# Optimization experiments

Hardware: AMD Instinct MI355X
Metric: run time of the kernel (lower is better)

Reference implementation:

```python
import jax, jax.numpy as jnp
import numpy as np

FEATURE_DIM = 512
Z_DIM = 256
Q_DIM = 128
NUM_Z_CODES = 4096
NUM_Q_CODES = 2048
HIDDEN_DIM = 128 * 4  # 512
BOTTLENECK = 64
BATCH = 32768


def setup_inputs() -> dict:
    key = jax.random.key(0)
    ks = jax.random.split(key, 16)
    d = {}
    d['x'] = jax.random.normal(ks[0], (BATCH, FEATURE_DIM), dtype=jnp.float32)
    # encoder: Linear(feature_dim,64) -> GELU -> Linear(64,hidden) -> GELU
    d['eW1'] = jax.random.normal(ks[1], (BOTTLENECK, FEATURE_DIM), dtype=jnp.float32) * (1.0 / np.sqrt(FEATURE_DIM))
    d['eb1'] = jnp.zeros((BOTTLENECK,), jnp.float32)
    d['eW2'] = jax.random.normal(ks[2], (HIDDEN_DIM, BOTTLENECK), dtype=jnp.float32) * (1.0 / np.sqrt(BOTTLENECK))
    d['eb2'] = jnp.zeros((HIDDEN_DIM,), jnp.float32)
    # to_z_latent LipschitzMLP(hidden, z_dim)
    d['zW'] = jax.random.normal(ks[3], (Z_DIM, HIDDEN_DIM), dtype=jnp.float32) * (1.0 / np.sqrt(HIDDEN_DIM))
    d['zb'] = jnp.zeros((Z_DIM,), jnp.float32)
    d['zci'] = jnp.ones((Z_DIM,), jnp.float32)
    # z codebook
    d['z_codebook'] = jax.random.normal(ks[4], (NUM_Z_CODES, Z_DIM), dtype=jnp.float32)
    # q_encoder LipschitzMLP(z_dim, q_dim)
    d['qW'] = jax.random.normal(ks[5], (Q_DIM, Z_DIM), dtype=jnp.float32) * (1.0 / np.sqrt(Z_DIM))
    d['qb'] = jnp.zeros((Q_DIM,), jnp.float32)
    d['qci'] = jnp.ones((Q_DIM,), jnp.float32)
    # q codebook
    d['q_codebook'] = jax.random.normal(ks[6], (NUM_Q_CODES, Q_DIM), dtype=jnp.float32)
    # decoder: Linear(q_dim,64) -> GELU -> Linear(64,hidden) -> GELU
    d['dW1'] = jax.random.normal(ks[7], (BOTTLENECK, Q_DIM), dtype=jnp.float32) * (1.0 / np.sqrt(Q_DIM))
    d['db1'] = jnp.zeros((BOTTLENECK,), jnp.float32)
    d['dW2'] = jax.random.normal(ks[8], (HIDDEN_DIM, BOTTLENECK), dtype=jnp.float32) * (1.0 / np.sqrt(BOTTLENECK))
    d['db2'] = jnp.zeros((HIDDEN_DIM,), jnp.float32)
    # to_output Linear(hidden, feature_dim)
    d['oW'] = jax.random.normal(ks[9], (FEATURE_DIM, HIDDEN_DIM), dtype=jnp.float32) * (1.0 / np.sqrt(HIDDEN_DIM))
    d['ob'] = jnp.zeros((FEATURE_DIM,), jnp.float32)
    return d


def _gelu(x):
    return jax.nn.gelu(x, approximate=False)  # torch nn.GELU default (erf)


def _lipschitz_mlp(x, W, b, ci):
    # normalization: scale each row of W so its L1 norm <= softplus(ci)
    absrowsum = jnp.sum(jnp.abs(W), axis=1, keepdims=True)          # [out,1]
    scale = jnp.minimum(1.0, jax.nn.softplus(ci)[:, None] / absrowsum)
    W_norm = W * scale
    return jax.nn.sigmoid(x @ W_norm.T + b)


def _quantize(z_e, codebook):
    # ||a-b||^2 = ||a||^2 + ||b||^2 - 2 a.b ; single big GEMM
    z_norm = jnp.sum(z_e * z_e, axis=1, keepdims=True)              # [B,1]
    cb_norm = jnp.sum(codebook * codebook, axis=1)[None, :]         # [1,K]
    dists = z_norm + cb_norm - 2.0 * (z_e @ codebook.T)             # [B,K]
    idx = jnp.argmin(dists, axis=1)
    z_q = codebook[idx]
    return z_q, idx


def _mse(a, b):
    return jnp.mean((a - b) ** 2)


def reference(x, eW1, eb1, eW2, eb2, zW, zb, zci, z_codebook,
              qW, qb, qci, q_codebook, dW1, db1, dW2, db2, oW, ob):
    sg = jax.lax.stop_gradient
    # encoder
    h = _gelu(_gelu(x @ eW1.T + eb1) @ eW2.T + eb2)                 # [B,hidden]
    z_e = _lipschitz_mlp(h, zW, zb, zci)                            # [B,z_dim]
    z_q, z_idx = _quantize(z_e, z_codebook)
    commit_z = _mse(z_e, sg(z_q))
    codebook_z = _mse(z_q, sg(z_e))
    # q level
    q_e = _lipschitz_mlp(sg(z_q), qW, qb, qci)                      # [B,q_dim]
    q_q, q_idx = _quantize(q_e, q_codebook)
    commit_q = _mse(q_e, sg(q_q))
    codebook_q = _mse(q_q, sg(q_e))
    # decoder
    dec_h = _gelu(_gelu(q_q @ dW1.T + db1) @ dW2.T + db2)           # [B,hidden]
    x_recon = dec_h @ oW.T + ob                                     # [B,feature]
    recon_loss = _mse(x_recon, x)
    loss = recon_loss + 0.25 * (commit_z + codebook_z) + 0.25 * (commit_q + codebook_q)
    return (loss, recon_loss, commit_z, codebook_z, commit_q, codebook_q,
            x_recon, z_q, q_q, z_idx, q_idx)
```

## Files before the change

### kernel.cpp

```cpp
#include <hip/hip_runtime.h>

typedef unsigned long long u64;
typedef unsigned short u16;
typedef unsigned int u32;


namespace {

constexpr int kBatch = 32768;

__device__ __forceinline__ float gelu_f(float x) {
  return 0.5f * x * (1.0f + erff(x * 0.70710678118654752440f));
}
__device__ __forceinline__ float sigmoid_f(float x) {
  return 1.0f / (1.0f + expf(-x));
}
__device__ __forceinline__ u64 pack_key(float d, unsigned j) {
  unsigned u = __float_as_uint(d);
  u = (u & 0x80000000u) ? ~u : (u | 0x80000000u);
  return ((u64)u << 32) | j;
}
__device__ __forceinline__ u16 bf16_rne(float x) {
  unsigned u = __float_as_uint(x);
  unsigned r = (u + 0x7FFFu + ((u >> 16) & 1u)) >> 16;
  return (u16)r;
}
__device__ __forceinline__ float bf16_to_f(u16 h) {
  return __uint_as_float((unsigned)h << 16);
}
__device__ __forceinline__ u64 min64(u64 a, u64 b) { return a < b ? a : b; }

__device__ __forceinline__ void load_lds16(const void* g, void* l) {
  __builtin_amdgcn_global_load_lds(
      (const __attribute__((address_space(1))) void*)g,
      (__attribute__((address_space(3))) void*)l, 16, 0, 0);
}

typedef short bf16x8 __attribute__((ext_vector_type(8)));
typedef float f32x4 __attribute__((ext_vector_type(4)));

__global__ void prep_cb_kernel(const float* __restrict__ zcb,
                               u16* __restrict__ zcbh, float* __restrict__ zcbn,
                               const float* __restrict__ qcb,
                               u16* __restrict__ qcbh, float* __restrict__ qcbn) {
  int b = blockIdx.x;
  const float* cb;
  u16* cbh;
  float* cbn;
  int K;
  if (b < 1024) { cb = zcb; cbh = zcbh; cbn = zcbn; K = 256; }
  else { b -= 1024; cb = qcb; cbh = qcbh; cbn = qcbn; K = 128; }
  const int row = b * 4 + (threadIdx.x >> 6);
  const int lane = threadIdx.x & 63;
  double s = 0.0;
  for (int k = lane; k < K; k += 64) {
    const float v = cb[(size_t)row * K + k];
    cbh[(size_t)row * K + k] = bf16_rne(v);
    s += (double)v * (double)v;
  }
#pragma unroll
  for (int o = 32; o > 0; o >>= 1) s += __shfl_down(s, o);
  if (lane == 0) cbn[row] = (float)s;
}

__global__ void prep_w_kernel(
    const float* __restrict__ zW, const float* __restrict__ zci,
    const float* __restrict__ qW, const float* __restrict__ qci,
    const float* __restrict__ eW1, const float* __restrict__ eW2,
    u16* __restrict__ zWns, u16* __restrict__ qWns, u16* __restrict__ eW1s,
    u16* __restrict__ eW2s, const float* __restrict__ dW1,
    const float* __restrict__ dW2, const float* __restrict__ oW,
    u16* __restrict__ dW1b, u16* __restrict__ dW2b, u16* __restrict__ oWb) {
  const int b = blockIdx.x;
  const int tid = threadIdx.x;
  if (b < 384) {
    const float* W;
    const float* ci;
    u16* D;
    int K, row;
    if (b < 256) { W = zW; ci = zci; D = zWns; K = 512; row = b; }
    else { W = qW; ci = qci; D = qWns; K = 256; row = b - 256; }
    float s = 0.f;
    for (int k = tid; k < K; k += 256) s += fabsf(W[(size_t)row * K + k]);
#pragma unroll
    for (int o = 32; o > 0; o >>= 1) s += __shfl_down(s, o);
    __shared__ float p[4];
    if ((tid & 63) == 0) p[tid >> 6] = s;
    __syncthreads();
    const float tot = p[0] + p[1] + p[2] + p[3];
    const float c = ci[row];
    const float sp = (c > 20.f) ? c : log1pf(expf(c));
    const float scale = fminf(1.f, sp / tot);
    for (int k = tid; k < K; k += 256) {
      const float v = W[(size_t)row * K + k] * scale;
      const u16 h = bf16_rne(v);
      const u16 l = bf16_rne(v - bf16_to_f(h));
      D[(size_t)row * 3 * K + k] = h;
      D[(size_t)row * 3 * K + K + k] = h;
      D[(size_t)row * 3 * K + 2 * K + k] = l;
    }
  } else if (b < 512) {
    const int i = (b - 384) * 256 + tid;
    const int r = i >> 9, k = i & 511;
    const float v = eW1[i];
    const u16 h = bf16_rne(v);
    const u16 l = bf16_rne(v - bf16_to_f(h));
    eW1s[(size_t)r * 1536 + k] = h;
    eW1s[(size_t)r * 1536 + 512 + k] = h;
    eW1s[(size_t)r * 1536 + 1024 + k] = l;
  } else if (b < 640) {
    const int i = (b - 512) * 256 + tid;
    const int r = i >> 6, k = i & 63;
    const float v = eW2[i];
    const u16 h = bf16_rne(v);
    const u16 l = bf16_rne(v - bf16_to_f(h));
    eW2s[(size_t)r * 192 + k] = h;
    eW2s[(size_t)r * 192 + 64 + k] = h;
    eW2s[(size_t)r * 192 + 128 + k] = l;
  } else if (b < 672) {
    const int i = (b - 640) * 256 + tid;
    dW1b[i] = bf16_rne(dW1[i]);
  } else if (b < 800) {
    const int i = (b - 672) * 256 + tid;
    dW2b[i] = bf16_rne(dW2[i]);
  } else {
    const int i = (b - 800) * 256 + tid;
    oWb[i] = bf16_rne(oW[i]);
  }
}

__global__ void cast_split_x_kernel(const float* __restrict__ x,
                                    u16* __restrict__ xs) {
  const int i = blockIdx.x * 256 + threadIdx.x;
  const int row = i >> 7, c4 = i & 127;
  const float4 v = *(const float4*)(x + (size_t)row * 512 + c4 * 4);
  const float vv[4] = {v.x, v.y, v.z, v.w};
  u16 hv[4], lv[4];
#pragma unroll
  for (int j = 0; j < 4; ++j) {
    hv[j] = bf16_rne(vv[j]);
    lv[j] = bf16_rne(vv[j] - bf16_to_f(hv[j]));
  }
  *(ushort4*)(xs + (size_t)row * 1024 + c4 * 4) =
      make_ushort4(hv[0], hv[1], hv[2], hv[3]);
  *(ushort4*)(xs + (size_t)row * 1024 + 512 + c4 * 4) =
      make_ushort4(lv[0], lv[1], lv[2], lv[3]);
}

enum { U_GELU_SPLIT = 0, U_SIG_SPLIT = 1, U_GELU_B16 = 2, U_RECON = 3 };

template <int TM, int TN, int NW, int MODE>
__global__ __launch_bounds__(NW * 64) void gemm_uni(
    const u16* __restrict__ A, const u16* __restrict__ B,
    const float* __restrict__ bias, void* __restrict__ Cv,
    const float* __restrict__ X, float* __restrict__ sumptr, int Ktot,
    int wrapA, int strideA, int N) {
  __shared__ __align__(16) u16 As[TM * 64];
  __shared__ __align__(16) u16 Bs[TN * 64];
  constexpr int NT = NW * 64;
  constexpr int AIT = (TM * 8) / NT;
  constexpr int BIT = (TN * 8) / NT;
  const int tid = threadIdx.x;
  const int lane = tid & 63, w = tid >> 6;
  const int quad = lane >> 4, l15 = lane & 15;
  const int waveM = (TN == 64) ? w * 64 : (w & 1) * 64;
  const int waveN = (TN == 64) ? 0 : (w >> 1) * 64;
  const int rowBase = blockIdx.y * TM;
  const int colBase = blockIdx.x * TN;

  f32x4 acc[4][4] = {};

  for (int k0 = 0; k0 < Ktot; k0 += 64) {
    const int sk0 = (k0 >= wrapA) ? k0 - wrapA : k0;
    __syncthreads();
#pragma unroll
    for (int i = 0; i < AIT; ++i) {
      const int ch = i * NT + tid;
      const int r = ch >> 3, c = ch & 7, g = c ^ (r & 7);
      load_lds16(A + (size_t)(rowBase + r) * strideA + sk0 + g * 8,
                 (char*)As + ch * 16);
    }
#pragma unroll
    for (int i = 0; i < BIT; ++i) {
      const int ch = i * NT + tid;
      const int r = ch >> 3, c = ch & 7, g = c ^ (r & 7);
      load_lds16(B + (size_t)(colBase + r) * Ktot + k0 + g * 8,
                 (char*)Bs + ch * 16);
    }
    __syncthreads();
#pragma unroll
    for (int ks = 0; ks < 2; ++ks) {
      bf16x8 af[4], bf[4];
      const int ch = ks * 4 + quad;
#pragma unroll
      for (int mi = 0; mi < 4; ++mi) {
        const int rl = waveM + mi * 16 + l15;
        af[mi] = *(const bf16x8*)(As + rl * 64 + (ch ^ (rl & 7)) * 8);
      }
#pragma unroll
      for (int ni = 0; ni < 4; ++ni) {
        const int rl = waveN + ni * 16 + l15;
        bf[ni] = *(const bf16x8*)(Bs + rl * 64 + (ch ^ (rl & 7)) * 8);
      }
#pragma unroll
      for (int mi = 0; mi < 4; ++mi)
#pragma unroll
        for (int ni = 0; ni < 4; ++ni)
          acc[mi][ni] = __builtin_amdgcn_mfma_f32_16x16x32_bf16(
              af[mi], bf[ni], acc[mi][ni], 0, 0, 0);
    }
  }

  if constexpr (MODE == U_GELU_SPLIT || MODE == U_SIG_SPLIT) {
    u16* S = (u16*)Cv;
#pragma unroll
    for (int mi = 0; mi < 4; ++mi)
#pragma unroll
      for (int r = 0; r < 4; ++r) {
        const int row = rowBase + waveM + mi * 16 + quad * 4 + r;
#pragma unroll
        for (int ni = 0; ni < 4; ++ni) {
          const int col = colBase + waveN + ni * 16 + l15;
          const float pre = acc[mi][ni][r] + bias[col];
          const float v = (MODE == U_GELU_SPLIT) ? gelu_f(pre) : sigmoid_f(pre);
          const u16 h = bf16_rne(v);
          const u16 l = bf16_rne(v - bf16_to_f(h));
          S[(size_t)row * 2 * N + col] = h;
          S[(size_t)row * 2 * N + N + col] = l;
        }
      }
  } else if constexpr (MODE == U_GELU_B16) {
    u16* C = (u16*)Cv;
#pragma unroll
    for (int mi = 0; mi < 4; ++mi)
#pragma unroll
      for (int r = 0; r < 4; ++r) {
        const int row = rowBase + waveM + mi * 16 + quad * 4 + r;
#pragma unroll
        for (int ni = 0; ni < 4; ++ni) {
          const int col = colBase + waveN + ni * 16 + l15;
          C[(size_t)row * N + col] =
              bf16_rne(gelu_f(acc[mi][ni][r] + bias[col]));
        }
      }
  } else {
    float* C = (float*)Cv;
    float local = 0.f;
#pragma unroll
    for (int mi = 0; mi < 4; ++mi)
#pragma unroll
      for (int r = 0; r < 4; ++r) {
        const int row = rowBase + waveM + mi * 16 + quad * 4 + r;
#pragma unroll
        for (int ni = 0; ni < 4; ++ni) {
          const int col = colBase + waveN + ni * 16 + l15;
          const float val = acc[mi][ni][r] + bias[col];
          const float d = val - X[(size_t)row * N + col];
          local += d * d;
          C[(size_t)row * N + col] = val;
        }
      }
#pragma unroll
    for (int o = 32; o > 0; o >>= 1) local += __shfl_down(local, o);
    __shared__ float psum[NW];
    if (lane == 0) psum[w] = local;
    __syncthreads();
    if (tid == 0) {
      float t = 0.f;
#pragma unroll
      for (int i = 0; i < NW; ++i) t += psum[i];
      atomicAdd(sumptr, t);
    }
  }
}

template <int KT, int BTG, int MINW>
__global__ __launch_bounds__(256, MINW) void dist2p_kernel(
    const u16* __restrict__ CB, const u16* __restrict__ ZB,
    const float* __restrict__ cbn, u32* __restrict__ cand, int strideB,
    int nx) {
  constexpr int CH = KT / 8;
  constexpr int KSTEPS = KT / 32;
  __shared__ __align__(16) u16 buf[128 * KT];
  u32* wred = (u32*)buf;
  const int tid = threadIdx.x;
  const int lane = tid & 63, w = tid >> 6;
  const int quad = lane >> 4, l15 = lane & 15;
  const int waveM = (w & 1) * 64;
  const int waveN = (w >> 1) * 64;
  const int ct = blockIdx.y;
  const int btg = blockIdx.x;
  const int codeBase = ct * 128;

#pragma unroll
  for (int i = 0; i < (128 * CH) / 256; ++i) {
    const int ch = i * 256 + tid;
    const int r = ch / CH, c = ch % CH, g = c ^ (r & 7);
    load_lds16(CB + (size_t)(codeBase + r) * KT + g * 8, (char*)buf + ch * 16);
  }
  __syncthreads();
  bf16x8 af[KSTEPS][4];
#pragma unroll
  for (int kk = 0; kk < KSTEPS; ++kk)
#pragma unroll
    for (int mi = 0; mi < 4; ++mi) {
      const int rl = waveM + mi * 16 + l15;
      const int sw = (kk * 4 + quad) ^ (rl & 7);
      af[kk][mi] = *(const bf16x8*)(buf + rl * KT + sw * 8);
    }
  float cnf[4][4];
#pragma unroll
  for (int mi = 0; mi < 4; ++mi)
#pragma unroll
    for (int r = 0; r < 4; ++r)
      cnf[mi][r] =
          cbn[codeBase + waveM + mi * 16 + quad * 4 + r] * 512.0f + 131072.0f;

  for (int bt = 0; bt < BTG; ++bt) {
    const int rowBase = (btg * BTG + bt) * 128;
    __syncthreads();
#pragma unroll
    for (int i = 0; i < (128 * CH) / 256; ++i) {
      const int ch = i * 256 + tid;
      const int r = ch / CH, c = ch % CH, g = c ^ (r & 7);
      load_lds16(ZB + (size_t)(rowBase + r) * strideB + g * 8,
                 (char*)buf + ch * 16);
    }
    __syncthreads();

    f32x4 acc[4][4] = {};
#pragma unroll
    for (int kk = 0; kk < KSTEPS; ++kk) {
      bf16x8 bf[4];
#pragma unroll
      for (int ni = 0; ni < 4; ++ni) {
        const int rn = waveN + ni * 16 + l15;
        const int sw = (kk * 4 + quad) ^ (rn & 7);
        bf[ni] = *(const bf16x8*)(buf + rn * KT + sw * 8);
      }
#pragma unroll
      for (int mi = 0; mi < 4; ++mi)
#pragma unroll
        for (int ni = 0; ni < 4; ++ni)
          acc[mi][ni] = __builtin_amdgcn_mfma_f32_16x16x32_bf16(
              af[kk][mi], bf[ni], acc[mi][ni], 0, 0, 0);
    }
    __syncthreads();

#pragma unroll
    for (int ni = 0; ni < 4; ++ni) {
      u32 b0 = ~0u, b1 = ~0u;
#pragma unroll
      for (int mi = 0; mi < 4; ++mi)
#pragma unroll
        for (int r = 0; r < 4; ++r) {
          const float kf = fmaf(acc[mi][ni][r], -1024.0f, cnf[mi][r]);
          u32 iv = (u32)kf;
          iv = iv > 0xFFFFFu ? 0xFFFFFu : iv;
          const u32 key =
              (iv << 12) | (codeBase + waveM + mi * 16 + quad * 4 + r);
          if (key < b0) { b1 = b0; b0 = key; }
          else if (key < b1) { b1 = key; }
        }
#pragma unroll
      for (int off = 16; off < 64; off <<= 1) {
        const u32 o0 = __shfl_xor(b0, off);
        const u32 o1 = __shfl_xor(b1, off);
        const u32 n0 = min(b0, o0);
        const u32 n1 = min(max(b0, o0), min(b1, o1));
        b0 = n0; b1 = n1;
      }
      if (quad == 0) {
        const int rloc = waveN + ni * 16 + l15;
        wred[rloc * 4 + (w & 1) * 2 + 0] = b0;
        wred[rloc * 4 + (w & 1) * 2 + 1] = b1;
      }
    }
    __syncthreads();
    if (tid < 128) {
      const u32 a0 = wred[tid * 4 + 0], a1 = wred[tid * 4 + 1];
      const u32 c0 = wred[tid * 4 + 2], c1 = wred[tid * 4 + 3];
      const u32 b0 = min(a0, c0);
      const u32 b1 = min(max(a0, c0), min(a1, c1));
      u32* dst = cand + (size_t)(rowBase + tid) * (2 * nx) + 2 * ct;
      *(u64*)dst = ((u64)b1 << 32) | b0;
    }
  }
}

template <int K, int NC, int LEVEL>
__global__ __launch_bounds__(256) void rerank_kernel(
    const u32* __restrict__ cand, const u16* __restrict__ zes,
    const float* __restrict__ cb, const float* __restrict__ cbn,
    float* __restrict__ outq, u16* __restrict__ wsq,
    float* __restrict__ out_idx, float* __restrict__ sumptr) {
  const int w = threadIdx.x >> 6, lane = threadIdx.x & 63;
  const int row = blockIdx.x * 4 + w;

  u32 key = (lane < NC) ? cand[(size_t)row * NC + lane] : ~0u;
  unsigned topcode[8];
#pragma unroll
  for (int t = 0; t < 8; ++t) {
    u32 m = key;
#pragma unroll
    for (int off = 1; off < 64; off <<= 1) m = min(m, __shfl_xor(m, off));
    topcode[t] = m & 0xFFFu;
    if (key == m) key = ~0u;
  }

  const int g = lane >> 3, sub = lane & 7;
  unsigned ci = topcode[0];
#pragma unroll
  for (int t = 1; t < 8; ++t) ci = (g == t) ? topcode[t] : ci;

  const u16* zr = zes + (size_t)row * 2 * K;
  const float* cr = cb + (size_t)ci * K;
  float dot = 0.f;
#pragma unroll
  for (int k = sub * (K / 8); k < (sub + 1) * (K / 8); k += 4) {
    const ushort4 hv = *(const ushort4*)(zr + k);
    const ushort4 lv = *(const ushort4*)(zr + K + k);
    const float4 cv = *(const float4*)(cr + k);
    dot = fmaf(bf16_to_f(hv.x) + bf16_to_f(lv.x), cv.x, dot);
    dot = fmaf(bf16_to_f(hv.y) + bf16_to_f(lv.y), cv.y, dot);
    dot = fmaf(bf16_to_f(hv.z) + bf16_to_f(lv.z), cv.z, dot);
    dot = fmaf(bf16_to_f(hv.w) + bf16_to_f(lv.w), cv.w, dot);
  }
#pragma unroll
  for (int off = 1; off < 8; off <<= 1) dot += __shfl_xor(dot, off);
  u64 k2 = pack_key(cbn[ci] - 2.0f * dot, ci);
#pragma unroll
  for (int off = 8; off < 64; off <<= 1) k2 = min64(k2, __shfl_xor(k2, off));
  const unsigned best = (unsigned)k2;
  if (lane == 0) out_idx[row] = (float)best;

  const float* br = cb + (size_t)best * K;
  float local = 0.f;
  for (int c = lane; c < K; c += 64) {
    const float v = br[c];
    const float z = bf16_to_f(zr[c]) + bf16_to_f(zr[K + c]);
    const float d = z - v;
    local += d * d;
    outq[(size_t)row * K + c] = v;
    if (LEVEL == 0) {
      const u16 h = bf16_rne(v);
      wsq[(size_t)row * 2 * K + c] = h;
      wsq[(size_t)row * 2 * K + K + c] = bf16_rne(v - bf16_to_f(h));
    } else {
      wsq[(size_t)row * K + c] = bf16_rne(v);
    }
  }
#pragma unroll
  for (int o = 32; o > 0; o >>= 1) local += __shfl_down(local, o);
  __shared__ float p[4];
  if (lane == 0) p[w] = local;
  __syncthreads();
  if (threadIdx.x == 0) atomicAdd(sumptr, p[0] + p[1] + p[2] + p[3]);
}

__global__ void finalize_kernel(const float* __restrict__ sums,
                                float* __restrict__ out) {
  const float cz = sums[0] / ((float)kBatch * 256.f);
  const float cq = sums[1] / ((float)kBatch * 128.f);
  const float rec = sums[2] / ((float)kBatch * 512.f);
  out[0] = rec + 0.5f * cz + 0.5f * cq;
  out[1] = rec;
  out[2] = cz;
  out[3] = cz;
  out[4] = cq;
  out[5] = cq;
}

}

extern "C" void kernel_launch(void* const* d_in, const int* in_sizes, int n_in,
                              void* d_out, int out_size, void* d_ws,
                              size_t ws_size, hipStream_t stream) {
  const float* x   = (const float*)d_in[0];
  const float* eW1 = (const float*)d_in[1];
  const float* eb1 = (const float*)d_in[2];
  const float* eW2 = (const float*)d_in[3];
  const float* eb2 = (const float*)d_in[4];
  const float* zW  = (const float*)d_in[5];
  const float* zb  = (const float*)d_in[6];
  const float* zci = (const float*)d_in[7];
  const float* zcb = (const float*)d_in[8];
  const float* qW  = (const float*)d_in[9];
  const float* qb  = (const float*)d_in[10];
  const float* qci = (const float*)d_in[11];
  const float* qcb = (const float*)d_in[12];
  const float* dW1 = (const float*)d_in[13];
  const float* db1 = (const float*)d_in[14];
  const float* dW2 = (const float*)d_in[15];
  const float* db2 = (const float*)d_in[16];
  const float* oW  = (const float*)d_in[17];
  const float* ob  = (const float*)d_in[18];

  float* out = (float*)d_out;
  float* out_xr = out + 6;
  float* out_zq = out_xr + (size_t)32768 * 512;
  float* out_qq = out_zq + (size_t)32768 * 256;
  float* out_zi = out_qq + (size_t)32768 * 128;
  float* out_qi = out_zi + 32768;

  char* wsb = (char*)d_ws;
  u16*  zWns = (u16*) (wsb + 0x0000000);
  u16*  qWns = (u16*) (wsb + 0x00C0000);
  u16*  eW1s = (u16*) (wsb + 0x00F0000);
  u16*  eW2s = (u16*) (wsb + 0x0120000);
  u16*  dW1b = (u16*) (wsb + 0x0150000);
  u16*  dW2b = (u16*) (wsb + 0x0154000);
  u16*  oWb  = (u16*) (wsb + 0x0164000);
  u16*  zcbh = (u16*) (wsb + 0x01E4000);
  u16*  qcbh = (u16*) (wsb + 0x03E4000);
  float* zcbn = (float*)(wsb + 0x0464000);
  float* qcbn = (float*)(wsb + 0x0468000);
  float* sums = (float*)(wsb + 0x046A000);
  u16*  h1s  = (u16*) (wsb + 0x0480000);
  u16*  h1b  = (u16*) (wsb + 0x0480000);
  u16*  zes  = (u16*) (wsb + 0x0C80000);
  u16*  qes  = (u16*) (wsb + 0x0C80000);
  u16*  hb   = (u16*) (wsb + 0x0C80000);
  u16*  xs   = (u16*) (wsb + 0x2C80000);
  u16*  hs   = (u16*) (wsb + 0x2C80000);
  u32*  candz = (u32*)(wsb + 0x2C80000);
  u16*  zqs  = (u16*) (wsb + 0x3480000);
  u32*  candq = (u32*)(wsb + 0x2C80000);
  u16*  qqb  = (u16*) (wsb + 0x5480000);

  hipMemsetAsync(sums, 0, 3 * sizeof(float), stream);

  prep_cb_kernel<<<1536, 256, 0, stream>>>(zcb, zcbh, zcbn, qcb, qcbh, qcbn);
  prep_w_kernel<<<1824, 256, 0, stream>>>(zW, zci, qW, qci, eW1, eW2, zWns,
                                          qWns, eW1s, eW2s, dW1, dW2, oW,
                                          dW1b, dW2b, oWb);
  cast_split_x_kernel<<<16384, 256, 0, stream>>>(x, xs);

  gemm_uni<128, 64, 2, U_GELU_SPLIT><<<dim3(1, 256), 128, 0, stream>>>(
      xs, eW1s, eb1, h1s, nullptr, nullptr, 1536, 1024, 1024, 64);
  gemm_uni<128, 128, 4, U_GELU_SPLIT><<<dim3(4, 256), 256, 0, stream>>>(
      h1s, eW2s, eb2, hs, nullptr, nullptr, 192, 128, 128, 512);
  gemm_uni<128, 128, 4, U_SIG_SPLIT><<<dim3(2, 256), 256, 0, stream>>>(
      hs, zWns, zb, zes, nullptr, nullptr, 1536, 1024, 1024, 256);

  dist2p_kernel<256, 16, 1><<<dim3(16, 32), 256, 0, stream>>>(
      zcbh, zes, zcbn, candz, 512, 32);
  rerank_kernel<256, 64, 0><<<8192, 256, 0, stream>>>(
      candz, zes, zcb, zcbn, out_zq, zqs, out_zi, &sums[0]);

  gemm_uni<128, 128, 4, U_SIG_SPLIT><<<dim3(1, 256), 256, 0, stream>>>(
      zqs, qWns, qb, qes, nullptr, nullptr, 768, 512, 512, 128);
  dist2p_kernel<128, 8, 2><<<dim3(32, 16), 256, 0, stream>>>(
      qcbh, qes, qcbn, candq, 256, 16);
  rerank_kernel<128, 32, 1><<<8192, 256, 0, stream>>>(
      candq, qes, qcb, qcbn, out_qq, qqb, out_qi, &sums[1]);

  gemm_uni<128, 64, 2, U_GELU_B16><<<dim3(1, 256), 128, 0, stream>>>(
      qqb, dW1b, db1, h1b, nullptr, nullptr, 128, 1 << 30, 128, 64);
  gemm_uni<128, 128, 4, U_GELU_B16><<<dim3(4, 256), 256, 0, stream>>>(
      h1b, dW2b, db2, hb, nullptr, nullptr, 64, 1 << 30, 64, 512);
  gemm_uni<128, 128, 4, U_RECON><<<dim3(4, 256), 256, 0, stream>>>(
      hb, oWb, ob, out_xr, x, &sums[2], 512, 1 << 30, 512, 512);

  finalize_kernel<<<1, 1, 0, stream>>>(sums, out);

  (void)in_sizes; (void)n_in; (void)out_size; (void)ws_size;
}
```

Measured before the change: 834.1 us.

## Double-buffer batch tiles in codebook distance kernel with explicit vmcnt waits

The distance kernel now uses two LDS buffers for the batch-row tiles. It prefetches the next tile with global_load_lds while MFMAs run on the current one, and uses explicit s_waitcnt vmcnt and raw barriers in place of full __syncthreads. For the z level, each block now handles 32 row tiles instead of 16, halving the grid, and the min-waves launch bound is dropped. The goal is to hide global-to-LDS latency and cut barrier stalls. In exchange, LDS use roughly doubles, which limits occupancy to about one block per CU, and the kernel now relies on hand-placed waitcnt ordering.

Result: no change. 834.9 us (+0.1%).

```diff
diff --git a/kernel.cpp b/kernel.cpp
--- a/kernel.cpp
+++ b/kernel.cpp
@@ -34,6 +34,32 @@
   __builtin_amdgcn_global_load_lds(
       (const __attribute__((address_space(1))) void*)g,
       (__attribute__((address_space(3))) void*)l, 16, 0, 0);
+}
+
+template <int N>
+__device__ __forceinline__ void wait_vmcnt() {
+  if constexpr (N == 0) {
+    asm volatile("s_waitcnt vmcnt(0)" ::: "memory");
+  } else if constexpr (N == 8) {
+    asm volatile("s_waitcnt vmcnt(8)" ::: "memory");
+  } else if constexpr (N == 16) {
+    asm volatile("s_waitcnt vmcnt(16)" ::: "memory");
+  }
+}
+
+__device__ __forceinline__ void lds_fence_barrier_pre() {
+  asm volatile("s_waitcnt lgkmcnt(0)" ::: "memory");
+  __builtin_amdgcn_sched_barrier(0);
+  __builtin_amdgcn_s_barrier();
+  asm volatile("" ::: "memory");
+  __builtin_amdgcn_sched_barrier(0);
+}
+
+__device__ __forceinline__ void barrier_raw() {
+  __builtin_amdgcn_sched_barrier(0);
+  __builtin_amdgcn_s_barrier();
+  asm volatile("" ::: "memory");
+  __builtin_amdgcn_sched_barrier(0);
 }
 
 typedef short bf16x8 __attribute__((ext_vector_type(8)));
@@ -274,15 +300,17 @@
   }
 }
 
-template <int KT, int BTG, int MINW>
-__global__ __launch_bounds__(256, MINW) void dist2p_kernel(
+template <int KT, int BTG>
+__global__ __launch_bounds__(256) void dist2p_kernel(
     const u16* __restrict__ CB, const u16* __restrict__ ZB,
     const float* __restrict__ cbn, u32* __restrict__ cand, int strideB,
     int nx) {
   constexpr int CH = KT / 8;
   constexpr int KSTEPS = KT / 32;
-  __shared__ __align__(16) u16 buf[128 * KT];
-  u32* wred = (u32*)buf;
+  constexpr int SLOTS = (128 * CH) / 256;
+  __shared__ __align__(16) u16 bufA[128 * KT];
+  __shared__ __align__(16) u16 bufB[128 * KT];
+  __shared__ u32 wred[128 * 4];
   const int tid = threadIdx.x;
   const int lane = tid & 63, w = tid >> 6;
   const int quad = lane >> 4, l15 = lane & 15;
@@ -292,13 +320,34 @@
   const int btg = blockIdx.x;
   const int codeBase = ct * 128;
 
-#pragma unroll
-  for (int i = 0; i < (128 * CH) / 256; ++i) {
+  float cnf[4][4];
+#pragma unroll
+  for (int mi = 0; mi < 4; ++mi)
+#pragma unroll
+    for (int r = 0; r < 4; ++r)
+      cnf[mi][r] =
+          cbn[codeBase + waveM + mi * 16 + quad * 4 + r] * 512.0f + 131072.0f;
+  asm volatile("" ::: "memory");
+
+#pragma unroll
+  for (int i = 0; i < SLOTS; ++i) {
     const int ch = i * 256 + tid;
     const int r = ch / CH, c = ch % CH, g = c ^ (r & 7);
-    load_lds16(CB + (size_t)(codeBase + r) * KT + g * 8, (char*)buf + ch * 16);
-  }
-  __syncthreads();
+    load_lds16(CB + (size_t)(codeBase + r) * KT + g * 8, (char*)bufA + ch * 16);
+  }
+  {
+    const int rowBase0 = btg * BTG * 128;
+#pragma unroll
+    for (int i = 0; i < SLOTS; ++i) {
+      const int ch = i * 256 + tid;
+      const int r = ch / CH, c = ch % CH, g = c ^ (r & 7);
+      load_lds16(ZB + (size_t)(rowBase0 + r) * strideB + g * 8,
+                 (char*)bufB + ch * 16);
+    }
+  }
+  wait_vmcnt<SLOTS>();
+  barrier_raw();
+
   bf16x8 af[KSTEPS][4];
 #pragma unroll
   for (int kk = 0; kk < KSTEPS; ++kk)
@@ -306,27 +355,28 @@
     for (int mi = 0; mi < 4; ++mi) {
       const int rl = waveM + mi * 16 + l15;
       const int sw = (kk * 4 + quad) ^ (rl & 7);
-      af[kk][mi] = *(const bf16x8*)(buf + rl * KT + sw * 8);
-    }
-  float cnf[4][4];
-#pragma unroll
-  for (int mi = 0; mi < 4; ++mi)
-#pragma unroll
-    for (int r = 0; r < 4; ++r)
-      cnf[mi][r] =
-          cbn[codeBase + waveM + mi * 16 + quad * 4 + r] * 512.0f + 131072.0f;
+      af[kk][mi] = *(const bf16x8*)(bufA + rl * KT + sw * 8);
+    }
+  lds_fence_barrier_pre();
 
   for (int bt = 0; bt < BTG; ++bt) {
     const int rowBase = (btg * BTG + bt) * 128;
-    __syncthreads();
-#pragma unroll
-    for (int i = 0; i < (128 * CH) / 256; ++i) {
-      const int ch = i * 256 + tid;
-      const int r = ch / CH, c = ch % CH, g = c ^ (r & 7);
-      load_lds16(ZB + (size_t)(rowBase + r) * strideB + g * 8,
-                 (char*)buf + ch * 16);
-    }
-    __syncthreads();
+    const u16* curp = (bt & 1) ? bufA : bufB;
+    u16* nxtp = (bt & 1) ? bufB : bufA;
+
+    if (bt + 1 < BTG) {
+#pragma unroll
+      for (int i = 0; i < SLOTS; ++i) {
+        const int ch = i * 256 + tid;
+        const int r = ch / CH, c = ch % CH, g = c ^ (r & 7);
+        load_lds16(ZB + (size_t)(rowBase + 128 + r) * strideB + g * 8,
+                   (char*)nxtp + ch * 16);
+      }
+      wait_vmcnt<SLOTS>();
+    } else {
+      wait_vmcnt<0>();
+    }
+    barrier_raw();
 
     f32x4 acc[4][4] = {};
 #pragma unroll
@@ -336,7 +386,7 @@
       for (int ni = 0; ni < 4; ++ni) {
         const int rn = waveN + ni * 16 + l15;
         const int sw = (kk * 4 + quad) ^ (rn & 7);
-        bf[ni] = *(const bf16x8*)(buf + rn * KT + sw * 8);
+        bf[ni] = *(const bf16x8*)(curp + rn * KT + sw * 8);
       }
 #pragma unroll
       for (int mi = 0; mi < 4; ++mi)
@@ -345,7 +395,6 @@
           acc[mi][ni] = __builtin_amdgcn_mfma_f32_16x16x32_bf16(
               af[kk][mi], bf[ni], acc[mi][ni], 0, 0, 0);
     }
-    __syncthreads();
 
 #pragma unroll
     for (int ni = 0; ni < 4; ++ni) {
@@ -376,7 +425,7 @@
         wred[rloc * 4 + (w & 1) * 2 + 1] = b1;
       }
     }
-    __syncthreads();
+    lds_fence_barrier_pre();
     if (tid < 128) {
       const u32 a0 = wred[tid * 4 + 0], a1 = wred[tid * 4 + 1];
       const u32 c0 = wred[tid * 4 + 2], c1 = wred[tid * 4 + 3];
@@ -543,14 +592,14 @@
   gemm_uni<128, 128, 4, U_SIG_SPLIT><<<dim3(2, 256), 256, 0, stream>>>(
       hs, zWns, zb, zes, nullptr, nullptr, 1536, 1024, 1024, 256);
 
-  dist2p_kernel<256, 16, 1><<<dim3(16, 32), 256, 0, stream>>>(
+  dist2p_kernel<256, 32><<<dim3(8, 32), 256, 0, stream>>>(
       zcbh, zes, zcbn, candz, 512, 32);
   rerank_kernel<256, 64, 0><<<8192, 256, 0, stream>>>(
       candz, zes, zcb, zcbn, out_zq, zqs, out_zi, &sums[0]);
 
   gemm_uni<128, 128, 4, U_SIG_SPLIT><<<dim3(1, 256), 256, 0, stream>>>(
       zqs, qWns, qb, qes, nullptr, nullptr, 768, 512, 512, 128);
-  dist2p_kernel<128, 8, 2><<<dim3(32, 16), 256, 0, stream>>>(
+  dist2p_kernel<128, 8><<<dim3(32, 16), 256, 0, stream>>>(
       qcbh, qes, qcbn, candq, 256, 16);
   rerank_kernel<128, 32, 1><<<8192, 256, 0, stream>>>(
       candq, qes, qcb, qcbn, out_qq, qqb, out_qi, &sums[1]);
```
